# Performance work log

Hardware: AMD Instinct MI355X
Metric: run time of the kernel (lower is better)

## Reference

```python
import jax, jax.numpy as jnp
import numpy as np
from math import sqrt

D_MODEL = 768
N_HEADS = 12
D_K = 64
D_V = 64
LN_EPS = 1e-5
NEG = -1e9


def layer_norm(x, g, b):
    mu = jnp.mean(x, axis=-1, keepdims=True)
    var = jnp.mean((x - mu) ** 2, axis=-1, keepdims=True)
    return (x - mu) * jax.lax.rsqrt(var + LN_EPS) * g + b


def setup_inputs() -> dict:
    key = jax.random.key(0)
    ks = jax.random.split(key, 8)
    B, S = 4, 1024
    pro1 = jax.random.normal(ks[0], (B, S, D_MODEL), dtype=jnp.float32)
    pro2 = jax.random.normal(ks[1], (B, S, D_MODEL), dtype=jnp.float32)
    # attn_mask is [B, H, S2, S1]; transpose(2,3) masks scores [B,H,S1,S2]
    mask1_2 = jax.random.bernoulli(ks[2], 0.3, (B, N_HEADS, S, S))
    sc = 1.0 / np.sqrt(D_MODEL)
    W_Q = jax.random.normal(ks[3], (D_MODEL, D_K * N_HEADS), dtype=jnp.float32) * sc
    W_K = jax.random.normal(ks[4], (D_MODEL, D_K * N_HEADS), dtype=jnp.float32) * sc
    fc1 = jax.random.normal(ks[5], (D_V * N_HEADS, D_MODEL), dtype=jnp.float32) * sc
    g1 = jnp.ones((D_MODEL,), jnp.float32)
    b1 = jnp.zeros((D_MODEL,), jnp.float32)
    g2 = jnp.ones((D_MODEL,), jnp.float32)
    b2 = jnp.zeros((D_MODEL,), jnp.float32)
    return {"pro1": pro1, "pro2": pro2, "mask1_2": mask1_2,
            "W_Q": W_Q, "W_K": W_K, "fc1": fc1,
            "g1": g1, "b1": b1, "g2": g2, "b2": b2}


def reference(pro1, pro2, mask1_2, W_Q, W_K, fc1, g1, b1, g2, b2):
    B, S1, _ = pro1.shape
    S2 = pro2.shape[1]
    # project and split heads: [B, H, S, d_k]
    Q = (pro1 @ W_Q).reshape(B, S1, N_HEADS, D_K).transpose(0, 2, 1, 3)
    K = (pro2 @ W_K).reshape(B, S2, N_HEADS, D_K).transpose(0, 2, 1, 3)
    scores = jnp.einsum('bhsd,bhtd->bhst', Q, K) / sqrt(D_K)  # [B,H,S1,S2]
    mask = jnp.swapaxes(mask1_2, 2, 3)  # attn_mask.transpose(2,3)
    scores = jnp.where(mask, NEG, scores)
    attn1 = jax.nn.softmax(scores, axis=-1)                  # over S2
    attn2 = jax.nn.softmax(jnp.swapaxes(scores, -1, -2), axis=-1)  # over S1
    ctx1 = jnp.einsum('bhst,bhtd->bhsd', attn1, K)  # [B,H,S1,d_k]
    ctx2 = jnp.einsum('bhts,bhsd->bhtd', attn2, Q)  # [B,H,S2,d_k]
    c1 = ctx1.transpose(0, 2, 1, 3).reshape(B, S1, N_HEADS * D_V)
    c2 = ctx2.transpose(0, 2, 1, 3).reshape(B, S2, N_HEADS * D_V)
    # NOTE: original applies fc1 to BOTH branches (fc2 is dead code)
    o1 = layer_norm(c1 @ fc1, g1, b1)
    o2 = layer_norm(c2 @ fc1, g2, b2)
    return (o1, o2)
```

## Files before the change

### kernel.cpp

```cpp
#include <hip/hip_runtime.h>
#include <hip/hip_bf16.h>
#include <stdint.h>

#define S 1024
#define DMODEL 768
#define NH 12
#define DK 64
#define BB 4
#define BH 48
#define M4 4096

typedef __attribute__((ext_vector_type(8))) short bf16x8;
typedef __attribute__((ext_vector_type(4))) float f32x4;
typedef __attribute__((ext_vector_type(4))) _Float16 f16x4;
typedef __attribute__((ext_vector_type(8))) _Float16 f16x8;

static __device__ __forceinline__ unsigned short f2bf(float f) {
  unsigned int u = __float_as_uint(f);
  unsigned int r = u + 0x7FFFu + ((u >> 16) & 1u);
  return (unsigned short)(r >> 16);
}
static __device__ __forceinline__ bf16x8 ldfrag(const unsigned short* p) {
  uint4 q = *reinterpret_cast<const uint4*>(p);
  return __builtin_bit_cast(bf16x8, q);
}
static __device__ __forceinline__ f16x8 ldfragh(const unsigned short* p) {
  uint4 q = *reinterpret_cast<const uint4*>(p);
  return __builtin_bit_cast(f16x8, q);
}
static __device__ __forceinline__ unsigned short h2u(_Float16 h) {
  return __builtin_bit_cast(unsigned short, h);
}
static __device__ __forceinline__ f16x4 pack4(const float* p) {
  auto lo = __builtin_amdgcn_cvt_pkrtz(p[0], p[1]);
  auto hi = __builtin_amdgcn_cvt_pkrtz(p[2], p[3]);
  uint2 u;
  u.x = __builtin_bit_cast(unsigned int, lo);
  u.y = __builtin_bit_cast(unsigned int, hi);
  return __builtin_bit_cast(f16x4, u);
}
static __device__ __forceinline__ void gl2lds16(const unsigned short* g, unsigned short* l) {
  __builtin_amdgcn_global_load_lds(
      (const __attribute__((address_space(1))) unsigned int*)g,
      (__attribute__((address_space(3))) unsigned int*)l, 16, 0, 0);
}

__global__ __launch_bounds__(256) void k_convert(const float* __restrict__ i0, const float* __restrict__ i1,
                                                 unsigned short* __restrict__ o0, unsigned short* __restrict__ o1,
                                                 int n4) {
  const float* in = blockIdx.y ? i1 : i0;
  unsigned short* out = blockIdx.y ? o1 : o0;
  int i = blockIdx.x * 256 + threadIdx.x;
  if (i < n4) {
    float4 v = reinterpret_cast<const float4*>(in)[i];
    ushort4 o;
    o.x = f2bf(v.x); o.y = f2bf(v.y); o.z = f2bf(v.z); o.w = f2bf(v.w);
    reinterpret_cast<ushort4*>(out)[i] = o;
  }
}

__global__ __launch_bounds__(256) void k_transpose(const float* w0, const float* w1, const float* w2,
                                                   unsigned short* o0, unsigned short* o1, unsigned short* o2) {
  const float* in = blockIdx.z == 0 ? w0 : (blockIdx.z == 1 ? w1 : w2);
  unsigned short* out = blockIdx.z == 0 ? o0 : (blockIdx.z == 1 ? o1 : o2);
  __shared__ float tile[32][33];
  int n0 = blockIdx.x * 32, k0 = blockIdx.y * 32;
  int tid = threadIdx.x;
  int r = tid >> 3, c = (tid & 7) * 4;
  float4 v = *reinterpret_cast<const float4*>(in + (size_t)(k0 + r) * DMODEL + n0 + c);
  tile[r][c] = v.x; tile[r][c + 1] = v.y; tile[r][c + 2] = v.z; tile[r][c + 3] = v.w;
  __syncthreads();
  ushort4 o;
  o.x = f2bf(tile[c + 0][r]);
  o.y = f2bf(tile[c + 1][r]);
  o.z = f2bf(tile[c + 2][r]);
  o.w = f2bf(tile[c + 3][r]);
  *reinterpret_cast<ushort4*>(out + (size_t)(n0 + r) * DMODEL + k0 + c) = o;
}

__global__ __launch_bounds__(256) void k_pack(const int* __restrict__ mask,
                                              unsigned int* __restrict__ mp2) {
  int bh = blockIdx.y;
  int w = threadIdx.x >> 6, lane = threadIdx.x & 63;
  int tile = blockIdx.x * 4 + w;
  int rowg = tile >> 2, colg = tile & 3;
  int t0 = rowg * 64;
  const int* mb = mask + (size_t)bh * S * S + colg * 256;
  unsigned long long b0 = 0, b1 = 0, b2 = 0, b3 = 0;
#pragma unroll 8
  for (int r = 0; r < 64; ++r) {
    int4 v = *reinterpret_cast<const int4*>(mb + (size_t)(t0 + r) * S + lane * 4);
    unsigned long long c0 = __ballot(v.x != 0);
    unsigned long long c1 = __ballot(v.y != 0);
    unsigned long long c2 = __ballot(v.z != 0);
    unsigned long long c3 = __ballot(v.w != 0);
    if (lane == r) { b0 = c0; b1 = c1; b2 = c2; b3 = c3; }
  }
  unsigned int* p2 = mp2 + (size_t)bh * 32 * S + (size_t)(colg * 8) * S + t0 + lane;
  p2[(size_t)0 * S] = (unsigned)b0;  p2[(size_t)1 * S] = (unsigned)(b0 >> 32);
  p2[(size_t)2 * S] = (unsigned)b1;  p2[(size_t)3 * S] = (unsigned)(b1 >> 32);
  p2[(size_t)4 * S] = (unsigned)b2;  p2[(size_t)5 * S] = (unsigned)(b2 >> 32);
  p2[(size_t)6 * S] = (unsigned)b3;  p2[(size_t)7 * S] = (unsigned)(b3 >> 32);
}

__global__ __launch_bounds__(256, 3) void k_gemm(
    int mode,
    const unsigned short* __restrict__ A0, const unsigned short* __restrict__ A1,
    const unsigned short* __restrict__ Bt0, const unsigned short* __restrict__ Bt1,
    unsigned short* __restrict__ oQ0, unsigned short* __restrict__ oQ1,
    unsigned short* __restrict__ oT0, unsigned short* __restrict__ oT1,
    unsigned short* __restrict__ oH0, unsigned short* __restrict__ oH1) {
  const unsigned short* A = blockIdx.z ? A1 : A0;
  const unsigned short* Bt = blockIdx.z ? Bt1 : Bt0;
  __shared__ __align__(16) unsigned short As[128 * 64];
  __shared__ __align__(16) unsigned short Bs[128 * 64];
  int tid = threadIdx.x;
  int m0 = blockIdx.x * 128, n0 = blockIdx.y * 128;
  int w = tid >> 6, lane = tid & 63, lane15 = lane & 15, quad = lane >> 4;
  int row0 = (w >> 1) * 64, col0 = (w & 1) * 64;
  f32x4 acc[4][4] = {};

  const unsigned short* gA[4];
  const unsigned short* gB[4];
  unsigned short* lA[4];
  unsigned short* lB[4];
  {
    int lr = lane >> 3;
    int ch = lane & 7;
#pragma unroll
    for (int i = 0; i < 4; ++i) {
      int r = w * 32 + i * 8 + lr;
      int cs = ((ch ^ (r & 7)) * 8);
      gA[i] = A + (size_t)(m0 + r) * DMODEL + cs;
      gB[i] = Bt + (size_t)(n0 + r) * DMODEL + cs;
      lA[i] = &As[(w * 32 + i * 8) * 64];
      lB[i] = &Bs[(w * 32 + i * 8) * 64];
    }
  }
  int l7 = lane15 & 7;
#pragma unroll
  for (int i = 0; i < 4; ++i) { gl2lds16(gA[i], lA[i]); gl2lds16(gB[i], lB[i]); }

  for (int kc = 0; kc < 12; ++kc) {
    __syncthreads();
#pragma unroll
    for (int ks = 0; ks < 2; ++ks) {
      int co = (((ks * 4 + quad) ^ l7) * 8);
      bf16x8 a[4], b[4];
#pragma unroll
      for (int i = 0; i < 4; ++i) a[i] = ldfrag(&As[(row0 + i * 16 + lane15) * 64 + co]);
#pragma unroll
      for (int j = 0; j < 4; ++j) b[j] = ldfrag(&Bs[(col0 + j * 16 + lane15) * 64 + co]);
#pragma unroll
      for (int i = 0; i < 4; ++i)
#pragma unroll
        for (int j = 0; j < 4; ++j)
          acc[i][j] = __builtin_amdgcn_mfma_f32_16x16x32_bf16(a[i], b[j], acc[i][j], 0, 0, 0);
    }
    __syncthreads();
    if (kc < 11) {
      int ko = (kc + 1) * 64;
#pragma unroll
      for (int i = 0; i < 4; ++i) { gl2lds16(gA[i] + ko, lA[i]); gl2lds16(gB[i] + ko, lB[i]); }
    }
  }

  if (mode == 0) {
    unsigned short* out = blockIdx.z ? oQ1 : oQ0;
    unsigned short* outT = blockIdx.z ? oT1 : oT0;
    f16x4 iden;
#pragma unroll
    for (int i = 0; i < 4; ++i) iden[i] = (_Float16)((quad * 4 + i) == lane15 ? 1.0f : 0.0f);
    f32x4 zero4 = {};
#pragma unroll
    for (int i = 0; i < 4; ++i)
#pragma unroll
      for (int j = 0; j < 4; ++j) {
        f16x4 cf;
#pragma unroll
        for (int reg = 0; reg < 4; ++reg) cf[reg] = (_Float16)acc[i][j][reg];
        f32x4 tq = __builtin_amdgcn_mfma_f32_16x16x16f16(cf, iden, zero4, 0, 0, 0);
        {
          int m = m0 + row0 + i * 16 + lane15;
          int n = n0 + col0 + j * 16 + quad * 4;
          int b = m >> 10, s = m & 1023, h = n >> 6, d = n & 63;
          ushort4 o;
          o.x = h2u((_Float16)tq[0]); o.y = h2u((_Float16)tq[1]);
          o.z = h2u((_Float16)tq[2]); o.w = h2u((_Float16)tq[3]);
          *reinterpret_cast<ushort4*>(&out[(((size_t)(b * NH + h)) * S + s) * DK + d]) = o;
        }
        {
          int n = n0 + col0 + j * 16 + lane15;
          int m = m0 + row0 + i * 16 + quad * 4;
          int b = m >> 10, s = m & 1023, h = n >> 6, d = n & 63;
          ushort4 o;
          o.x = h2u((_Float16)acc[i][j][0]); o.y = h2u((_Float16)acc[i][j][1]);
          o.z = h2u((_Float16)acc[i][j][2]); o.w = h2u((_Float16)acc[i][j][3]);
          *reinterpret_cast<ushort4*>(&outT[(((size_t)(b * NH + h)) * DK + d) * S + s]) = o;
        }
      }
  } else {
    unsigned short* outh = blockIdx.z ? oH1 : oH0;
#pragma unroll
    for (int i = 0; i < 4; ++i)
#pragma unroll
      for (int j = 0; j < 4; ++j)
#pragma unroll
        for (int reg = 0; reg < 4; ++reg) {
          int m = m0 + row0 + i * 16 + quad * 4 + reg;
          int n = n0 + col0 + j * 16 + lane15;
          outh[(size_t)m * DMODEL + n] = h2u((_Float16)acc[i][j][reg]);
        }
  }
}

__global__ __launch_bounds__(256, 3) void k_attn(
    const unsigned short* __restrict__ Qb, const unsigned short* __restrict__ Kb,
    const unsigned short* __restrict__ QT, const unsigned short* __restrict__ KT,
    const unsigned int* __restrict__ mp2,
    unsigned short* __restrict__ c1, unsigned short* __restrict__ c2) {
  int lin = blockIdx.x;
  int xcd = lin & 7, idx = lin >> 3;
  int grp = xcd * 12 + (idx >> 3);
  int sb = idx & 7;
  int path = grp >= 48 ? 1 : 0;
  int bh = grp - path * 48;
  int s0b = sb * 128;

  const unsigned short* X = path ? Kb : Qb;
  const unsigned short* Y = path ? Qb : Kb;
  const unsigned short* YT = path ? QT : KT;
  unsigned short* outc = path ? c2 : c1;

  __shared__ __align__(16) unsigned short YS[2][64 * 72];
  __shared__ __align__(16) unsigned short YTS[2][64 * 72];
  __shared__ __align__(16) unsigned int MWS[2][512];

  const unsigned short* Xb = X + (size_t)bh * S * DK;
  const unsigned short* Yb = Y + (size_t)bh * S * DK;
  const unsigned short* YTb = YT + (size_t)bh * DK * S;
  const unsigned int* mbg = mp2 + (size_t)bh * 32 * S;

  int tid = threadIdx.x;
  int w = tid >> 6, lane = tid & 63, lane15 = lane & 15, quad = lane >> 4;
  int s0w = s0b + w * 32;
  int ck = lane15 & 3;
  int sh0 = w * 8 + (lane15 >> 2);

  f16x8 xf[2][2];
#pragma unroll
  for (int rg = 0; rg < 2; ++rg) {
    xf[rg][0] = ldfragh(Xb + (size_t)(s0w + rg * 16 + lane15) * DK + quad * 8);
    xf[rg][1] = ldfragh(Xb + (size_t)(s0w + rg * 16 + lane15) * DK + 32 + quad * 8);
  }

  int sr4 = tid >> 2, sc4 = (tid & 3) * 16;
  const unsigned short* gY = Yb + (size_t)sr4 * DK + sc4;
  const unsigned short* gYT = YTb + (size_t)sr4 * S + sc4;
  uint4 y0 = *reinterpret_cast<const uint4*>(gY);
  uint4 y1 = *reinterpret_cast<const uint4*>(gY + 8);
  uint4 t0 = *reinterpret_cast<const uint4*>(gYT);
  uint4 t1 = *reinterpret_cast<const uint4*>(gYT + 8);

  int mj = tid >> 2;
  int p0wi = (sb >> 1) * 8 + (tid & 3) * 2 + (sb & 1);
  int tl = tid >> 1;
  int k0 = (tid & 1) * 2, k1 = k0 + 1;
  unsigned mwv0, mwv1 = 0;
  if (path == 0) {
    mwv0 = mbg[(size_t)p0wi * S + mj];
  } else {
    mwv0 = mbg[(size_t)(k0 * 2) * S + s0b + tl];
    mwv1 = mbg[(size_t)(k1 * 2) * S + s0b + tl];
  }

  f32x4 outa[2][4] = {};
  float lsum[2] = {0.f, 0.f};

  for (int jc = 0; jc < 16; ++jc) {
    int buf = jc & 1;
    *reinterpret_cast<uint4*>(&YS[buf][sr4 * 72 + sc4]) = y0;
    *reinterpret_cast<uint4*>(&YS[buf][sr4 * 72 + sc4 + 8]) = y1;
    *reinterpret_cast<uint4*>(&YTS[buf][sr4 * 72 + sc4]) = t0;
    *reinterpret_cast<uint4*>(&YTS[buf][sr4 * 72 + sc4 + 8]) = t1;
    if (path == 0) {
      MWS[buf][tid] = mwv0;
    } else {
      uint2 mw; mw.x = mwv0; mw.y = mwv1;
      *reinterpret_cast<uint2*>(&MWS[buf][tid * 2]) = mw;
    }
    {
      int jcn = (jc + 1 < 16) ? jc + 1 : jc;
      int jn = jcn * 64;
      y0 = *reinterpret_cast<const uint4*>(gY + (size_t)jn * DK);
      y1 = *reinterpret_cast<const uint4*>(gY + (size_t)jn * DK + 8);
      t0 = *reinterpret_cast<const uint4*>(gYT + jn);
      t1 = *reinterpret_cast<const uint4*>(gYT + jn + 8);
      if (path == 0) {
        mwv0 = mbg[(size_t)p0wi * S + jn + mj];
      } else {
        size_t wb = (size_t)((jcn >> 2) * 8 + ((jcn >> 1) & 1)) * S + s0b + tl;
        mwv0 = mbg[wb + (size_t)(k0 * 2) * S];
        mwv1 = mbg[wb + (size_t)(k1 * 2) * S];
      }
    }
    __syncthreads();

    f32x4 scv[4][2];
#pragma unroll
    for (int st = 0; st < 4; ++st) {
      f16x8 a0 = ldfragh(&YS[buf][(st * 16 + lane15) * 72 + quad * 8]);
      f16x8 a1 = ldfragh(&YS[buf][(st * 16 + lane15) * 72 + 32 + quad * 8]);
#pragma unroll
      for (int rg = 0; rg < 2; ++rg) {
        f32x4 v = {};
        v = __builtin_amdgcn_mfma_f32_16x16x32_f16(a0, xf[rg][0], v, 0, 0, 0);
        v = __builtin_amdgcn_mfma_f32_16x16x32_f16(a1, xf[rg][1], v, 0, 0, 0);
        scv[st][rg] = v;
      }
    }
    f16x4 pfa[4][2];
    if (path == 0) {
#pragma unroll
      for (int st = 0; st < 4; ++st) {
        float pv[2][4];
#pragma unroll
        for (int reg = 0; reg < 4; ++reg) {
          unsigned wdv = MWS[buf][(st * 16 + quad * 4 + reg) * 4 + ck];
#pragma unroll
          for (int rg = 0; rg < 2; ++rg) {
            float e = __expf(scv[st][rg][reg] * 0.125f);
            float p = ((wdv >> (unsigned)(sh0 + rg * 4)) & 1u) ? 0.f : e;
            lsum[rg] += p;
            pv[rg][reg] = p;
          }
        }
        pfa[st][0] = pack4(pv[0]);
        pfa[st][1] = pack4(pv[1]);
      }
    } else {
#pragma unroll
      for (int rg = 0; rg < 2; ++rg) {
        int bidx = (w * 32 + rg * 16 + lane15) * 4;
        uint4 wq = *reinterpret_cast<const uint4*>(&MWS[buf][bidx]);
        unsigned wd4[4] = {wq.x, wq.y, wq.z, wq.w};
#pragma unroll
        for (int st = 0; st < 4; ++st) {
          float pv[4];
          unsigned shb = (unsigned)((jc & 1) * 16 + st * 4 + quad);
#pragma unroll
          for (int reg = 0; reg < 4; ++reg) {
            float e = __expf(scv[st][rg][reg] * 0.125f);
            float p = ((wd4[reg] >> shb) & 1u) ? 0.f : e;
            lsum[rg] += p;
            pv[reg] = p;
          }
          pfa[st][rg] = pack4(pv);
        }
      }
    }
#pragma unroll
    for (int st = 0; st < 4; ++st)
#pragma unroll
      for (int dsub = 0; dsub < 4; ++dsub) {
        uint2 q = *reinterpret_cast<const uint2*>(&YTS[buf][(dsub * 16 + lane15) * 72 + st * 16 + quad * 4]);
        f16x4 yb = __builtin_bit_cast(f16x4, q);
#pragma unroll
        for (int rg = 0; rg < 2; ++rg)
          outa[rg][dsub] = __builtin_amdgcn_mfma_f32_16x16x16f16(pfa[st][rg], yb, outa[rg][dsub], 0, 0, 0);
      }
  }

#pragma unroll
  for (int rg = 0; rg < 2; ++rg) {
    lsum[rg] += __shfl_xor(lsum[rg], 16);
    lsum[rg] += __shfl_xor(lsum[rg], 32);
  }
  float rinv[2][4];
#pragma unroll
  for (int rg = 0; rg < 2; ++rg)
#pragma unroll
    for (int reg = 0; reg < 4; ++reg)
      rinv[rg][reg] = 1.0f / __shfl(lsum[rg], quad * 4 + reg);

  int b = bh / NH, h = bh % NH;
#pragma unroll
  for (int rg = 0; rg < 2; ++rg)
#pragma unroll
    for (int dsub = 0; dsub < 4; ++dsub)
#pragma unroll
      for (int reg = 0; reg < 4; ++reg) {
        float v = outa[rg][dsub][reg] * rinv[rg][reg];
        int srow = s0w + rg * 16 + quad * 4 + reg;
        size_t idxo = ((size_t)(b * S) + srow) * DMODEL + h * DK + dsub * 16 + lane15;
        outc[idxo] = f2bf(v);
      }
}

__global__ __launch_bounds__(256) void k_ln(const unsigned short* __restrict__ f1,
                                            const unsigned short* __restrict__ f2,
                                            const float* __restrict__ g1, const float* __restrict__ b1,
                                            const float* __restrict__ g2, const float* __restrict__ b2,
                                            float* __restrict__ out) {
  int rowg = blockIdx.x;
  int sel = rowg >> 12;
  int row = rowg & 4095;
  const unsigned short* in = sel ? f2 : f1;
  const float* g = sel ? g2 : g1;
  const float* be = sel ? b2 : b1;
  int tid = threadIdx.x;
  const unsigned short* p = in + (size_t)row * DMODEL;
  float x0 = (float)__builtin_bit_cast(_Float16, p[tid]);
  float x1 = (float)__builtin_bit_cast(_Float16, p[tid + 256]);
  float x2 = (float)__builtin_bit_cast(_Float16, p[tid + 512]);
  float s = x0 + x1 + x2;
  float ss = x0 * x0 + x1 * x1 + x2 * x2;
#pragma unroll
  for (int m = 1; m < 64; m <<= 1) { s += __shfl_xor(s, m); ss += __shfl_xor(ss, m); }
  __shared__ float ps[4], pss[4];
  int w = tid >> 6;
  if ((tid & 63) == 0) { ps[w] = s; pss[w] = ss; }
  __syncthreads();
  s = ps[0] + ps[1] + ps[2] + ps[3];
  ss = pss[0] + pss[1] + pss[2] + pss[3];
  float mu = s * (1.0f / 768.0f);
  float var = ss * (1.0f / 768.0f) - mu * mu;
  float rstd = rsqrtf(var + 1e-5f);
  float* o = out + ((size_t)sel * M4 + row) * DMODEL;
  o[tid] = (x0 - mu) * rstd * g[tid] + be[tid];
  o[tid + 256] = (x1 - mu) * rstd * g[tid + 256] + be[tid + 256];
  o[tid + 512] = (x2 - mu) * rstd * g[tid + 512] + be[tid + 512];
}

extern "C" void kernel_launch(void* const* d_in, const int* in_sizes, int n_in,
                              void* d_out, int out_size, void* d_ws, size_t ws_size,
                              hipStream_t stream) {
  const float* pro1 = (const float*)d_in[0];
  const float* pro2 = (const float*)d_in[1];
  const int* mask = (const int*)d_in[2];
  const float* WQ = (const float*)d_in[3];
  const float* WK = (const float*)d_in[4];
  const float* FC1 = (const float*)d_in[5];
  const float* g1 = (const float*)d_in[6];
  const float* b1 = (const float*)d_in[7];
  const float* g2 = (const float*)d_in[8];
  const float* b2 = (const float*)d_in[9];
  float* out = (float*)d_out;
  char* ws = (char*)d_ws;

  unsigned short* pro1b = (unsigned short*)(ws + 0);
  unsigned short* pro2b = (unsigned short*)(ws + 6291456);
  unsigned short* f1h = (unsigned short*)(ws + 0);
  unsigned short* wqt = (unsigned short*)(ws + 12582912);
  unsigned short* wkt = (unsigned short*)(ws + 13762560);
  unsigned short* fc1t = (unsigned short*)(ws + 14942208);
  unsigned short* Qb = (unsigned short*)(ws + 16121856);
  unsigned short* Kb = (unsigned short*)(ws + 22413312);
  unsigned short* QT = (unsigned short*)(ws + 28704768);
  unsigned short* KT = (unsigned short*)(ws + 34996224);
  unsigned int* mp2 = (unsigned int*)(ws + 41287680);
  unsigned short* f2h = (unsigned short*)(ws + 47579136);
  unsigned short* c1 = (unsigned short*)(ws + 60162048);
  unsigned short* c2 = (unsigned short*)(ws + 66453504);

  k_convert<<<dim3(3072, 2), 256, 0, stream>>>(pro1, pro2, pro1b, pro2b, 786432);
  k_transpose<<<dim3(24, 24, 3), 256, 0, stream>>>(WQ, WK, FC1, wqt, wkt, fc1t);
  k_pack<<<dim3(16, BH), 256, 0, stream>>>(mask, mp2);
  k_gemm<<<dim3(32, 6, 2), 256, 0, stream>>>(0, pro1b, pro2b, wqt, wkt,
                                             Qb, Kb, QT, KT, nullptr, nullptr);
  k_attn<<<dim3(768), 256, 0, stream>>>(Qb, Kb, QT, KT, mp2, c1, c2);
  k_gemm<<<dim3(32, 6, 2), 256, 0, stream>>>(1, c1, c2, fc1t, fc1t,
                                             nullptr, nullptr, nullptr, nullptr, f1h, f2h);
  k_ln<<<8192, 256, 0, stream>>>(f1h, f2h, g1, b1, g2, b2, out);
}
```

Baseline: 416.6 us.

## Fuse input conversion into GEMM, merge prep kernels, shrink GEMM tile, add setprio

The separate fp32-to-bf16 conversion kernel is removed. The projection GEMM now loads fp32 activations directly, packs them with v_cvt_pk_bf16_f32 and writes them into LDS, prefetching the next K chunk into registers. The weight-transpose and mask-pack kernels are merged into a single launch. GEMM tiles shrink to 64x128, which doubles the grid, and s_setprio hints are added around the MFMA phases of the attention kernel. The intent is to cut kernel launches and the bf16 intermediate round trip through memory, at the cost of a smaller per-block tile and more register pressure. A mask-word index in the attention kernel also changes.

```diff
diff --git a/kernel.cpp b/kernel.cpp
--- a/kernel.cpp
+++ b/kernel.cpp
@@ -20,6 +20,11 @@
   unsigned int r = u + 0x7FFFu + ((u >> 16) & 1u);
   return (unsigned short)(r >> 16);
 }
+static __device__ __forceinline__ unsigned pkbf(float a, float b) {
+  unsigned r;
+  asm("v_cvt_pk_bf16_f32 %0, %1, %2" : "=v"(r) : "v"(a), "v"(b));
+  return r;
+}
 static __device__ __forceinline__ bf16x8 ldfrag(const unsigned short* p) {
   uint4 q = *reinterpret_cast<const uint4*>(p);
   return __builtin_bit_cast(bf16x8, q);
@@ -45,123 +50,165 @@
       (__attribute__((address_space(3))) unsigned int*)l, 16, 0, 0);
 }
 
-__global__ __launch_bounds__(256) void k_convert(const float* __restrict__ i0, const float* __restrict__ i1,
-                                                 unsigned short* __restrict__ o0, unsigned short* __restrict__ o1,
-                                                 int n4) {
-  const float* in = blockIdx.y ? i1 : i0;
-  unsigned short* out = blockIdx.y ? o1 : o0;
-  int i = blockIdx.x * 256 + threadIdx.x;
-  if (i < n4) {
-    float4 v = reinterpret_cast<const float4*>(in)[i];
+__global__ __launch_bounds__(256) void k_prep(const float* __restrict__ w0, const float* __restrict__ w1,
+                                              const float* __restrict__ w2,
+                                              unsigned short* __restrict__ o0, unsigned short* __restrict__ o1,
+                                              unsigned short* __restrict__ o2,
+                                              const int* __restrict__ mask, unsigned int* __restrict__ mp2) {
+  int bid = blockIdx.x;
+  int tid = threadIdx.x;
+  if (bid < 1728) {
+    int z = bid / 576;
+    int r2 = bid - z * 576;
+    int bx = r2 % 24, by = r2 / 24;
+    const float* in = z == 0 ? w0 : (z == 1 ? w1 : w2);
+    unsigned short* out = z == 0 ? o0 : (z == 1 ? o1 : o2);
+    __shared__ float tile[32][33];
+    int n0 = bx * 32, k0 = by * 32;
+    int r = tid >> 3, c = (tid & 7) * 4;
+    float4 v = *reinterpret_cast<const float4*>(in + (size_t)(k0 + r) * DMODEL + n0 + c);
+    tile[r][c] = v.x; tile[r][c + 1] = v.y; tile[r][c + 2] = v.z; tile[r][c + 3] = v.w;
+    __syncthreads();
     ushort4 o;
-    o.x = f2bf(v.x); o.y = f2bf(v.y); o.z = f2bf(v.z); o.w = f2bf(v.w);
-    reinterpret_cast<ushort4*>(out)[i] = o;
-  }
-}
-
-__global__ __launch_bounds__(256) void k_transpose(const float* w0, const float* w1, const float* w2,
-                                                   unsigned short* o0, unsigned short* o1, unsigned short* o2) {
-  const float* in = blockIdx.z == 0 ? w0 : (blockIdx.z == 1 ? w1 : w2);
-  unsigned short* out = blockIdx.z == 0 ? o0 : (blockIdx.z == 1 ? o1 : o2);
-  __shared__ float tile[32][33];
-  int n0 = blockIdx.x * 32, k0 = blockIdx.y * 32;
-  int tid = threadIdx.x;
-  int r = tid >> 3, c = (tid & 7) * 4;
-  float4 v = *reinterpret_cast<const float4*>(in + (size_t)(k0 + r) * DMODEL + n0 + c);
-  tile[r][c] = v.x; tile[r][c + 1] = v.y; tile[r][c + 2] = v.z; tile[r][c + 3] = v.w;
-  __syncthreads();
-  ushort4 o;
-  o.x = f2bf(tile[c + 0][r]);
-  o.y = f2bf(tile[c + 1][r]);
-  o.z = f2bf(tile[c + 2][r]);
-  o.w = f2bf(tile[c + 3][r]);
-  *reinterpret_cast<ushort4*>(out + (size_t)(n0 + r) * DMODEL + k0 + c) = o;
-}
-
-__global__ __launch_bounds__(256) void k_pack(const int* __restrict__ mask,
-                                              unsigned int* __restrict__ mp2) {
-  int bh = blockIdx.y;
-  int w = threadIdx.x >> 6, lane = threadIdx.x & 63;
-  int tile = blockIdx.x * 4 + w;
-  int rowg = tile >> 2, colg = tile & 3;
-  int t0 = rowg * 64;
-  const int* mb = mask + (size_t)bh * S * S + colg * 256;
-  unsigned long long b0 = 0, b1 = 0, b2 = 0, b3 = 0;
+    o.x = f2bf(tile[c + 0][r]);
+    o.y = f2bf(tile[c + 1][r]);
+    o.z = f2bf(tile[c + 2][r]);
+    o.w = f2bf(tile[c + 3][r]);
+    *reinterpret_cast<ushort4*>(out + (size_t)(n0 + r) * DMODEL + k0 + c) = o;
+  } else {
+    int pb = bid - 1728;
+    int bh = pb >> 4;
+    int px = pb & 15;
+    int w = tid >> 6, lane = tid & 63;
+    int tile4 = px * 4 + w;
+    int rowg = tile4 >> 2, colg = tile4 & 3;
+    int t0 = rowg * 64;
+    const int* mb = mask + (size_t)bh * S * S + colg * 256;
+    unsigned long long b0 = 0, b1 = 0, b2 = 0, b3 = 0;
 #pragma unroll 8
-  for (int r = 0; r < 64; ++r) {
-    int4 v = *reinterpret_cast<const int4*>(mb + (size_t)(t0 + r) * S + lane * 4);
-    unsigned long long c0 = __ballot(v.x != 0);
-    unsigned long long c1 = __ballot(v.y != 0);
-    unsigned long long c2 = __ballot(v.z != 0);
-    unsigned long long c3 = __ballot(v.w != 0);
-    if (lane == r) { b0 = c0; b1 = c1; b2 = c2; b3 = c3; }
-  }
-  unsigned int* p2 = mp2 + (size_t)bh * 32 * S + (size_t)(colg * 8) * S + t0 + lane;
-  p2[(size_t)0 * S] = (unsigned)b0;  p2[(size_t)1 * S] = (unsigned)(b0 >> 32);
-  p2[(size_t)2 * S] = (unsigned)b1;  p2[(size_t)3 * S] = (unsigned)(b1 >> 32);
-  p2[(size_t)4 * S] = (unsigned)b2;  p2[(size_t)5 * S] = (unsigned)(b2 >> 32);
-  p2[(size_t)6 * S] = (unsigned)b3;  p2[(size_t)7 * S] = (unsigned)(b3 >> 32);
+    for (int r = 0; r < 64; ++r) {
+      int4 v = *reinterpret_cast<const int4*>(mb + (size_t)(t0 + r) * S + lane * 4);
+      unsigned long long c0 = __ballot(v.x != 0);
+      unsigned long long c1 = __ballot(v.y != 0);
+      unsigned long long c2 = __ballot(v.z != 0);
+      unsigned long long c3 = __ballot(v.w != 0);
+      if (lane == r) { b0 = c0; b1 = c1; b2 = c2; b3 = c3; }
+    }
+    unsigned int* p2 = mp2 + (size_t)bh * 32 * S + (size_t)(colg * 8) * S + t0 + lane;
+    p2[(size_t)0 * S] = (unsigned)b0;  p2[(size_t)1 * S] = (unsigned)(b0 >> 32);
+    p2[(size_t)2 * S] = (unsigned)b1;  p2[(size_t)3 * S] = (unsigned)(b1 >> 32);
+    p2[(size_t)4 * S] = (unsigned)b2;  p2[(size_t)5 * S] = (unsigned)(b2 >> 32);
+    p2[(size_t)6 * S] = (unsigned)b3;  p2[(size_t)7 * S] = (unsigned)(b3 >> 32);
+  }
 }
 
 __global__ __launch_bounds__(256, 3) void k_gemm(
     int mode,
+    const float* __restrict__ Af0, const float* __restrict__ Af1,
     const unsigned short* __restrict__ A0, const unsigned short* __restrict__ A1,
     const unsigned short* __restrict__ Bt0, const unsigned short* __restrict__ Bt1,
     unsigned short* __restrict__ oQ0, unsigned short* __restrict__ oQ1,
     unsigned short* __restrict__ oT0, unsigned short* __restrict__ oT1,
     unsigned short* __restrict__ oH0, unsigned short* __restrict__ oH1) {
-  const unsigned short* A = blockIdx.z ? A1 : A0;
   const unsigned short* Bt = blockIdx.z ? Bt1 : Bt0;
-  __shared__ __align__(16) unsigned short As[128 * 64];
+  __shared__ __align__(16) unsigned short As[64 * 64];
   __shared__ __align__(16) unsigned short Bs[128 * 64];
   int tid = threadIdx.x;
-  int m0 = blockIdx.x * 128, n0 = blockIdx.y * 128;
+  int m0 = blockIdx.x * 64, n0 = blockIdx.y * 128;
   int w = tid >> 6, lane = tid & 63, lane15 = lane & 15, quad = lane >> 4;
-  int row0 = (w >> 1) * 64, col0 = (w & 1) * 64;
-  f32x4 acc[4][4] = {};
-
-  const unsigned short* gA[4];
+  int col0 = w * 32;
+  f32x4 acc[4][2] = {};
+
   const unsigned short* gB[4];
-  unsigned short* lA[4];
   unsigned short* lB[4];
+  const unsigned short* gA[2];
+  unsigned short* lA[2];
   {
-    int lr = lane >> 3;
-    int ch = lane & 7;
+    int lr = lane >> 3, ch = lane & 7;
 #pragma unroll
     for (int i = 0; i < 4; ++i) {
       int r = w * 32 + i * 8 + lr;
       int cs = ((ch ^ (r & 7)) * 8);
-      gA[i] = A + (size_t)(m0 + r) * DMODEL + cs;
       gB[i] = Bt + (size_t)(n0 + r) * DMODEL + cs;
-      lA[i] = &As[(w * 32 + i * 8) * 64];
       lB[i] = &Bs[(w * 32 + i * 8) * 64];
     }
-  }
+    if (mode != 0) {
+      const unsigned short* A = blockIdx.z ? A1 : A0;
+#pragma unroll
+      for (int i = 0; i < 2; ++i) {
+        int r = w * 16 + i * 8 + lr;
+        int cs = ((ch ^ (r & 7)) * 8);
+        gA[i] = A + (size_t)(m0 + r) * DMODEL + cs;
+        lA[i] = &As[(w * 16 + i * 8) * 64];
+      }
+    }
+  }
+  int ar = tid >> 2, aj0 = (tid & 3) * 2;
+  const float* gAf = nullptr;
+  float4 af[4];
+  if (mode == 0) {
+    gAf = (blockIdx.z ? Af1 : Af0) + (size_t)(m0 + ar) * DMODEL + aj0 * 8;
+#pragma unroll
+    for (int q = 0; q < 4; ++q) af[q] = *reinterpret_cast<const float4*>(gAf + q * 4);
+  }
+  int arx = ar & 7;
+  unsigned short* lAw0 = &As[ar * 64 + ((aj0 ^ arx) * 8)];
+  unsigned short* lAw1 = &As[ar * 64 + (((aj0 + 1) ^ arx) * 8)];
+
+#pragma unroll
+  for (int i = 0; i < 4; ++i) gl2lds16(gB[i], lB[i]);
+  if (mode == 0) {
+    uint4 w0, w1;
+    w0.x = pkbf(af[0].x, af[0].y); w0.y = pkbf(af[0].z, af[0].w);
+    w0.z = pkbf(af[1].x, af[1].y); w0.w = pkbf(af[1].z, af[1].w);
+    w1.x = pkbf(af[2].x, af[2].y); w1.y = pkbf(af[2].z, af[2].w);
+    w1.z = pkbf(af[3].x, af[3].y); w1.w = pkbf(af[3].z, af[3].w);
+    *reinterpret_cast<uint4*>(lAw0) = w0;
+    *reinterpret_cast<uint4*>(lAw1) = w1;
+  } else {
+#pragma unroll
+    for (int i = 0; i < 2; ++i) gl2lds16(gA[i], lA[i]);
+  }
+
   int l7 = lane15 & 7;
-#pragma unroll
-  for (int i = 0; i < 4; ++i) { gl2lds16(gA[i], lA[i]); gl2lds16(gB[i], lB[i]); }
-
   for (int kc = 0; kc < 12; ++kc) {
     __syncthreads();
+    if (mode == 0 && kc < 11) {
+#pragma unroll
+      for (int q = 0; q < 4; ++q)
+        af[q] = *reinterpret_cast<const float4*>(gAf + (kc + 1) * 64 + q * 4);
+    }
 #pragma unroll
     for (int ks = 0; ks < 2; ++ks) {
       int co = (((ks * 4 + quad) ^ l7) * 8);
-      bf16x8 a[4], b[4];
-#pragma unroll
-      for (int i = 0; i < 4; ++i) a[i] = ldfrag(&As[(row0 + i * 16 + lane15) * 64 + co]);
-#pragma unroll
-      for (int j = 0; j < 4; ++j) b[j] = ldfrag(&Bs[(col0 + j * 16 + lane15) * 64 + co]);
+      bf16x8 a[4], b[2];
+#pragma unroll
+      for (int i = 0; i < 4; ++i) a[i] = ldfrag(&As[(i * 16 + lane15) * 64 + co]);
+#pragma unroll
+      for (int j = 0; j < 2; ++j) b[j] = ldfrag(&Bs[(col0 + j * 16 + lane15) * 64 + co]);
 #pragma unroll
       for (int i = 0; i < 4; ++i)
 #pragma unroll
-        for (int j = 0; j < 4; ++j)
+        for (int j = 0; j < 2; ++j)
           acc[i][j] = __builtin_amdgcn_mfma_f32_16x16x32_bf16(a[i], b[j], acc[i][j], 0, 0, 0);
     }
     __syncthreads();
     if (kc < 11) {
       int ko = (kc + 1) * 64;
 #pragma unroll
-      for (int i = 0; i < 4; ++i) { gl2lds16(gA[i] + ko, lA[i]); gl2lds16(gB[i] + ko, lB[i]); }
+      for (int i = 0; i < 4; ++i) gl2lds16(gB[i] + ko, lB[i]);
+      if (mode == 0) {
+        uint4 w0, w1;
+        w0.x = pkbf(af[0].x, af[0].y); w0.y = pkbf(af[0].z, af[0].w);
+        w0.z = pkbf(af[1].x, af[1].y); w0.w = pkbf(af[1].z, af[1].w);
+        w1.x = pkbf(af[2].x, af[2].y); w1.y = pkbf(af[2].z, af[2].w);
+        w1.z = pkbf(af[3].x, af[3].y); w1.w = pkbf(af[3].z, af[3].w);
+        *reinterpret_cast<uint4*>(lAw0) = w0;
+        *reinterpret_cast<uint4*>(lAw1) = w1;
+      } else {
+#pragma unroll
+        for (int i = 0; i < 2; ++i) gl2lds16(gA[i] + ko, lA[i]);
+      }
     }
   }
 
@@ -175,13 +222,13 @@
 #pragma unroll
     for (int i = 0; i < 4; ++i)
 #pragma unroll
-      for (int j = 0; j < 4; ++j) {
+      for (int j = 0; j < 2; ++j) {
         f16x4 cf;
 #pragma unroll
         for (int reg = 0; reg < 4; ++reg) cf[reg] = (_Float16)acc[i][j][reg];
         f32x4 tq = __builtin_amdgcn_mfma_f32_16x16x16f16(cf, iden, zero4, 0, 0, 0);
         {
-          int m = m0 + row0 + i * 16 + lane15;
+          int m = m0 + i * 16 + lane15;
           int n = n0 + col0 + j * 16 + quad * 4;
           int b = m >> 10, s = m & 1023, h = n >> 6, d = n & 63;
           ushort4 o;
@@ -191,7 +238,7 @@
         }
         {
           int n = n0 + col0 + j * 16 + lane15;
-          int m = m0 + row0 + i * 16 + quad * 4;
+          int m = m0 + i * 16 + quad * 4;
           int b = m >> 10, s = m & 1023, h = n >> 6, d = n & 63;
           ushort4 o;
           o.x = h2u((_Float16)acc[i][j][0]); o.y = h2u((_Float16)acc[i][j][1]);
@@ -204,10 +251,10 @@
 #pragma unroll
     for (int i = 0; i < 4; ++i)
 #pragma unroll
-      for (int j = 0; j < 4; ++j)
+      for (int j = 0; j < 2; ++j)
 #pragma unroll
         for (int reg = 0; reg < 4; ++reg) {
-          int m = m0 + row0 + i * 16 + quad * 4 + reg;
+          int m = m0 + i * 16 + quad * 4 + reg;
           int n = n0 + col0 + j * 16 + lane15;
           outh[(size_t)m * DMODEL + n] = h2u((_Float16)acc[i][j][reg]);
         }
@@ -297,7 +344,7 @@
       t0 = *reinterpret_cast<const uint4*>(gYT + jn);
       t1 = *reinterpret_cast<const uint4*>(gYT + jn + 8);
       if (path == 0) {
-        mwv0 = mbg[(size_t)p0wi * S + jn + mj];
+        mwv0 = mbg[(size_t)p0wi * S + jn + (tid >> 2)];
       } else {
         size_t wb = (size_t)((jcn >> 2) * 8 + ((jcn >> 1) & 1)) * S + s0b + tl;
         mwv0 = mbg[wb + (size_t)(k0 * 2) * S];
@@ -307,6 +354,7 @@
     __syncthreads();
 
     f32x4 scv[4][2];
+    __builtin_amdgcn_s_setprio(1);
 #pragma unroll
     for (int st = 0; st < 4; ++st) {
       f16x8 a0 = ldfragh(&YS[buf][(st * 16 + lane15) * 72 + quad * 8]);
@@ -319,6 +367,7 @@
         scv[st][rg] = v;
       }
     }
+    __builtin_amdgcn_s_setprio(0);
     f16x4 pfa[4][2];
     if (path == 0) {
 #pragma unroll
@@ -359,6 +408,7 @@
         }
       }
     }
+    __builtin_amdgcn_s_setprio(1);
 #pragma unroll
     for (int st = 0; st < 4; ++st)
 #pragma unroll
@@ -369,6 +419,7 @@
         for (int rg = 0; rg < 2; ++rg)
           outa[rg][dsub] = __builtin_amdgcn_mfma_f32_16x16x16f16(pfa[st][rg], yb, outa[rg][dsub], 0, 0, 0);
       }
+    __builtin_amdgcn_s_setprio(0);
   }
 
 #pragma unroll
@@ -448,8 +499,6 @@
   float* out = (float*)d_out;
   char* ws = (char*)d_ws;
 
-  unsigned short* pro1b = (unsigned short*)(ws + 0);
-  unsigned short* pro2b = (unsigned short*)(ws + 6291456);
   unsigned short* f1h = (unsigned short*)(ws + 0);
   unsigned short* wqt = (unsigned short*)(ws + 12582912);
   unsigned short* wkt = (unsigned short*)(ws + 13762560);
@@ -463,13 +512,11 @@
   unsigned short* c1 = (unsigned short*)(ws + 60162048);
   unsigned short* c2 = (unsigned short*)(ws + 66453504);
 
-  k_convert<<<dim3(3072, 2), 256, 0, stream>>>(pro1, pro2, pro1b, pro2b, 786432);
-  k_transpose<<<dim3(24, 24, 3), 256, 0, stream>>>(WQ, WK, FC1, wqt, wkt, fc1t);
-  k_pack<<<dim3(16, BH), 256, 0, stream>>>(mask, mp2);
-  k_gemm<<<dim3(32, 6, 2), 256, 0, stream>>>(0, pro1b, pro2b, wqt, wkt,
+  k_prep<<<2496, 256, 0, stream>>>(WQ, WK, FC1, wqt, wkt, fc1t, mask, mp2);
+  k_gemm<<<dim3(64, 6, 2), 256, 0, stream>>>(0, pro1, pro2, nullptr, nullptr, wqt, wkt,
                                              Qb, Kb, QT, KT, nullptr, nullptr);
   k_attn<<<dim3(768), 256, 0, stream>>>(Qb, Kb, QT, KT, mp2, c1, c2);
-  k_gemm<<<dim3(32, 6, 2), 256, 0, stream>>>(1, c1, c2, fc1t, fc1t,
+  k_gemm<<<dim3(64, 6, 2), 256, 0, stream>>>(1, nullptr, nullptr, c1, c2, fc1t, fc1t,
                                              nullptr, nullptr, nullptr, nullptr, f1h, f2h);
   k_ln<<<8192, 256, 0, stream>>>(f1h, f2h, g1, b1, g2, b2, out);
 }
```

New measurement: 415.8 us. No clear change (-0.2%).
